# Optimization experiments

Measured on AMD Instinct MI355X. Metric: run time of the kernel, lower is better.

Reference implementation:

```python
import jax, jax.numpy as jnp
import numpy as np

D_MODEL = 1024
N_HEADS = 16
HEAD_DIM = D_MODEL // N_HEADS


def setup_inputs() -> dict:
    key = jax.random.key(0)
    ks = jax.random.split(key, 5)
    B, T = 2, 2048
    x = jax.random.normal(ks[0], (B, T, D_MODEL), dtype=jnp.float32)
    s_in = 1.0 / np.sqrt(D_MODEL)
    W_qkv = jax.random.normal(ks[1], (D_MODEL, 3 * D_MODEL), dtype=jnp.float32) * s_in
    b_qkv = jnp.zeros((3 * D_MODEL,), dtype=jnp.float32)
    W_out = jax.random.normal(ks[2], (D_MODEL, D_MODEL), dtype=jnp.float32) * s_in
    b_out = jnp.zeros((D_MODEL,), dtype=jnp.float32)
    gamma = jnp.ones((D_MODEL,), dtype=jnp.float32)
    beta = jnp.zeros((D_MODEL,), dtype=jnp.float32)
    return {"x": x, "W_qkv": W_qkv, "b_qkv": b_qkv, "W_out": W_out,
            "b_out": b_out, "gamma": gamma, "beta": beta}


def _layernorm(x, gamma, beta, eps=1e-5):
    mu = jnp.mean(x, axis=-1, keepdims=True)
    var = jnp.var(x, axis=-1, keepdims=True)
    return (x - mu) * jax.lax.rsqrt(var + eps) * gamma + beta


def reference(x, W_qkv, b_qkv, W_out, b_out, gamma, beta):
    B, T, D = x.shape
    residual = x
    h = _layernorm(x, gamma, beta)
    qkv = h @ W_qkv + b_qkv                      # [B, T, 3D]
    qkv = qkv.reshape(B, T, 3, N_HEADS, HEAD_DIM)
    q = jnp.transpose(qkv[:, :, 0], (0, 2, 1, 3))  # [B, H, T, hd]
    k = jnp.transpose(qkv[:, :, 1], (0, 2, 1, 3))
    v = jnp.transpose(qkv[:, :, 2], (0, 2, 1, 3))
    scale = 1.0 / np.sqrt(HEAD_DIM)
    attn = jnp.einsum("bhqd,bhkd->bhqk", q, k) * scale
    attn = jax.nn.softmax(attn, axis=-1)
    out = jnp.einsum("bhqk,bhkd->bhqd", attn, v)   # [B, H, T, hd]
    out = jnp.transpose(out, (0, 2, 1, 3)).reshape(B, T, D)
    out = out @ W_out + b_out
    return residual + out
```

## Files before the change

kernel.cpp:

```cpp
#include <hip/hip_runtime.h>
#include <hip/hip_bf16.h>


#define DINL static __device__ __forceinline__

typedef __attribute__((ext_vector_type(8))) short bf16x8;
typedef __attribute__((ext_vector_type(4))) float f32x4;

DINL float fast_exp2(float x) { return __builtin_amdgcn_exp2f(x); }

DINL unsigned short f2bf(float f) {
  __hip_bfloat16 h = __float2bfloat16(f);
  unsigned short u;
  __builtin_memcpy(&u, &h, 2);
  return u;
}

DINL unsigned int bfbits(float f) {
  unsigned int u;
  __builtin_memcpy(&u, &f, 4);
  return (u + 0x8000u) >> 16;
}

DINL void gload_lds16(const void* g, void* l) {
  __builtin_amdgcn_global_load_lds((__attribute__((address_space(1))) void*)g,
                                   (__attribute__((address_space(3))) void*)l,
                                   16, 0, 0);
}

__global__ __launch_bounds__(256)
void ln_kernel(const float* __restrict__ x, const float* __restrict__ gamma,
               const float* __restrict__ beta, unsigned short* __restrict__ h) {
  __shared__ float red[8];
  int row = blockIdx.x;
  int t = threadIdx.x;
  float4 v = reinterpret_cast<const float4*>(x + (size_t)row * 1024)[t];
  float s  = v.x + v.y + v.z + v.w;
  float sq = v.x*v.x + v.y*v.y + v.z*v.z + v.w*v.w;
#pragma unroll
  for (int off = 1; off < 64; off <<= 1) {
    s  += __shfl_xor(s, off);
    sq += __shfl_xor(sq, off);
  }
  int wid = t >> 6;
  if ((t & 63) == 0) { red[wid] = s; red[4 + wid] = sq; }
  __syncthreads();
  s  = red[0] + red[1] + red[2] + red[3];
  sq = red[4] + red[5] + red[6] + red[7];
  float mu   = s * (1.0f / 1024.0f);
  float var  = sq * (1.0f / 1024.0f) - mu * mu;
  float rstd = rsqrtf(var + 1e-5f);
  float4 g = reinterpret_cast<const float4*>(gamma)[t];
  float4 b = reinterpret_cast<const float4*>(beta)[t];
  ushort4 o;
  o.x = f2bf((v.x - mu) * rstd * g.x + b.x);
  o.y = f2bf((v.y - mu) * rstd * g.y + b.y);
  o.z = f2bf((v.z - mu) * rstd * g.z + b.z);
  o.w = f2bf((v.w - mu) * rstd * g.w + b.w);
  reinterpret_cast<ushort4*>(h + (size_t)row * 1024)[t] = o;
}

__global__ __launch_bounds__(256)
void transpose_cast_kernel(const float* __restrict__ src, unsigned short* __restrict__ dst,
                           int R, int C) {
  __shared__ float tile[32][33];
  int tx = threadIdx.x & 31, ty = threadIdx.x >> 5;
  int c0 = blockIdx.x * 32, r0 = blockIdx.y * 32;
#pragma unroll
  for (int i = 0; i < 4; i++)
    tile[ty + i * 8][tx] = src[(size_t)(r0 + ty + i * 8) * C + c0 + tx];
  __syncthreads();
#pragma unroll
  for (int i = 0; i < 4; i++) {
    int r = ty + i * 8;
    dst[(size_t)(c0 + r) * R + r0 + tx] = f2bf(tile[tx][r]);
  }
}

template <int BM, int MODE>
__global__ __launch_bounds__(256)
void gemm128(const unsigned short* __restrict__ A,
             const unsigned short* __restrict__ Bt,
             int K,
             const float* __restrict__ bias,
             unsigned short* __restrict__ qdst, unsigned short* __restrict__ kdst,
             unsigned short* __restrict__ vTdst,
             const float* __restrict__ xres, float* __restrict__ out) {
  static_assert(BM == 128 || BM == 64, "");
  constexpr int MR = BM / 32;
  __shared__ unsigned short As[BM * 64];
  __shared__ unsigned short Bs[8192];
  int tid = threadIdx.x, wid = tid >> 6, lane = tid & 63;
  int l15 = lane & 15, l4 = lane >> 4;
  int brow = blockIdx.y * BM, bcol = blockIdx.x * 128;
  int wr = wid >> 1, wc = wid & 1;
  f32x4 acc[MR][4] = {};

  for (int kt = 0; kt < K; kt += 64) {
    __syncthreads();
#pragma unroll
    for (int r = 0; r < MR; r++) {
      int c  = wid * (BM * 2) + r * 64;
      int cl = c + lane;
      int kb = cl / BM, row = cl % BM;
      gload_lds16(A + (size_t)(brow + row) * K + kt + kb * 8, As + c * 8);
    }
#pragma unroll
    for (int r = 0; r < 4; r++) {
      int c  = wid * 256 + r * 64;
      int cl = c + lane;
      int kb = cl >> 7, row = cl & 127;
      gload_lds16(Bt + (size_t)(bcol + row) * K + kt + kb * 8, Bs + c * 8);
    }
    __syncthreads();
#pragma unroll
    for (int ks = 0; ks < 2; ks++) {
      int kb = ks * 4 + l4;
      bf16x8 af[MR], bfr[4];
#pragma unroll
      for (int m = 0; m < MR; m++)
        af[m] = *reinterpret_cast<const bf16x8*>(As + (kb * BM + wr * (BM / 2) + m * 16 + l15) * 8);
#pragma unroll
      for (int n = 0; n < 4; n++)
        bfr[n] = *reinterpret_cast<const bf16x8*>(Bs + (kb * 128 + wc * 64 + n * 16 + l15) * 8);
#pragma unroll
      for (int m = 0; m < MR; m++)
#pragma unroll
        for (int n = 0; n < 4; n++)
          acc[m][n] = __builtin_amdgcn_mfma_f32_16x16x32_bf16(af[m], bfr[n], acc[m][n], 0, 0, 0);
    }
  }

  if (MODE == 0) {
    int sec = bcol >> 10;
    int secbase = sec << 10;
#pragma unroll
    for (int m = 0; m < MR; m++) {
      int row0 = brow + wr * (BM / 2) + m * 16 + l4 * 4;
      int b = row0 >> 11, t0 = row0 & 2047;
#pragma unroll
      for (int n = 0; n < 4; n++) {
        int col = (bcol & 1023) + wc * 64 + n * 16 + l15;
        float bv = bias[secbase + col];
        int hh = col >> 6, d = col & 63;
        if (sec == 2) {
          ushort4 pk;
          pk.x = f2bf(acc[m][n][0] + bv);
          pk.y = f2bf(acc[m][n][1] + bv);
          pk.z = f2bf(acc[m][n][2] + bv);
          pk.w = f2bf(acc[m][n][3] + bv);
          *reinterpret_cast<ushort4*>(vTdst + ((size_t)(b * 16 + hh) * 64 + d) * 2048 + t0) = pk;
        } else {
          unsigned short* dst = (sec == 0) ? qdst : kdst;
          float sc = (sec == 0) ? 0.125f * 1.44269504088896f : 1.0f;
#pragma unroll
          for (int j = 0; j < 4; j++)
            dst[((size_t)(b * 16 + hh) * 2048 + t0 + j) * 64 + d] = f2bf((acc[m][n][j] + bv) * sc);
        }
      }
    }
  } else {
#pragma unroll
    for (int m = 0; m < MR; m++) {
      int row0 = brow + wr * (BM / 2) + m * 16 + l4 * 4;
#pragma unroll
      for (int n = 0; n < 4; n++) {
        int col = bcol + wc * 64 + n * 16 + l15;
        float bv = bias[col];
#pragma unroll
        for (int j = 0; j < 4; j++) {
          size_t idx = (size_t)(row0 + j) * 1024 + col;
          out[idx] = acc[m][n][j] + bv + xres[idx];
        }
      }
    }
  }
}

__global__ __launch_bounds__(256, 2)
void attn_kernel(const unsigned short* __restrict__ q,
                 const unsigned short* __restrict__ kk,
                 const unsigned short* __restrict__ vT,
                 unsigned short* __restrict__ o) {
  const int T = 2048;
  __shared__ unsigned short Ks[2][8192];
  __shared__ unsigned short Ps[4][2][2048];
  int tid = threadIdx.x, wid = tid >> 6, lane = tid & 63;
  int l15 = lane & 15, l4 = lane >> 4;
  int swz = (l15 & 7) << 3;

  int lin = blockIdx.x;
  int rl  = (lin & 7) * 64 + (lin >> 3);
  int bx = rl & 15, bh = rl >> 4;
  int q0 = bx * 128 + wid * 32;

  const unsigned short* qh = q  + (size_t)bh * T * 64;
  const unsigned short* kh = kk + (size_t)bh * T * 64;
  const unsigned short* vh = vT + (size_t)bh * 64 * T;

  bf16x8 qf[2][2];
#pragma unroll
  for (int m = 0; m < 2; m++)
#pragma unroll
    for (int ks = 0; ks < 2; ks++)
      qf[m][ks] = *reinterpret_cast<const bf16x8*>(
          qh + (size_t)(q0 + m * 16 + l15) * 64 + ks * 32 + l4 * 8);

  f32x4 accO[2][4] = {};
  float lst[2] = {0.0f, 0.0f};

#define STAGE128(buf, kv0)                                                     \
  {                                                                            \
    _Pragma("unroll") for (int r = 0; r < 4; r++) {                            \
      int c  = (wid * 4 + r) * 64;                                             \
      int cl = c + lane;                                                       \
      int key = cl >> 3;                                                       \
      int kb  = (cl & 7) ^ (key & 7);                                          \
      gload_lds16(kh + (size_t)((kv0) + key) * 64 + kb * 8, &Ks[buf][c * 8]);  \
    }                                                                          \
  }

#define QKSM(sub, par)                                                         \
  {                                                                            \
    f32x4 s[2][4] = {};                                                        \
    __builtin_amdgcn_s_setprio(1);                                             \
    _Pragma("unroll") for (int ks = 0; ks < 2; ks++) {                         \
      _Pragma("unroll") for (int n = 0; n < 4; n++) {                          \
        int kkey = (sub) * 64 + n * 16 + l15;                                  \
        int slot = kkey * 8 + ((ks * 4 + l4) ^ (kkey & 7));                    \
        bf16x8 kf = *reinterpret_cast<const bf16x8*>(&Ks[cur][slot * 8]);      \
        _Pragma("unroll") for (int m = 0; m < 2; m++)                          \
          s[m][n] = __builtin_amdgcn_mfma_f32_16x16x32_bf16(kf, qf[m][ks],     \
                                                            s[m][n], 0, 0, 0); \
      }                                                                        \
    }                                                                          \
    __builtin_amdgcn_s_setprio(0);                                             \
    _Pragma("unroll") for (int m = 0; m < 2; m++) {                            \
      float sum = 0.0f;                                                        \
      _Pragma("unroll") for (int n = 0; n < 4; n++) {                          \
        _Pragma("unroll") for (int j = 0; j < 4; j++) {                        \
          float p = fast_exp2(s[m][n][j]);                                     \
          s[m][n][j] = p;                                                      \
          sum += p;                                                            \
        }                                                                      \
        unsigned int u0 = bfbits(s[m][n][0]) | (bfbits(s[m][n][1]) << 16);     \
        unsigned int u1 = bfbits(s[m][n][2]) | (bfbits(s[m][n][3]) << 16);     \
        *reinterpret_cast<uint2*>(                                             \
            &Ps[wid][par][(m * 16 + l15) * 64 + ((n * 16 + l4 * 4) ^ swz)]) =  \
            make_uint2(u0, u1);                                                \
      }                                                                        \
      lst[m] += sum;                                                           \
    }                                                                          \
  }

#define PV(par, vf)                                                            \
  {                                                                            \
    __builtin_amdgcn_s_setprio(1);                                             \
    _Pragma("unroll") for (int ks = 0; ks < 2; ks++) {                         \
      _Pragma("unroll") for (int m = 0; m < 2; m++) {                          \
        bf16x8 pf = *reinterpret_cast<const bf16x8*>(                          \
            &Ps[wid][par][(m * 16 + l15) * 64 + ((ks * 32 + l4 * 8) ^ swz)]);  \
        _Pragma("unroll") for (int n = 0; n < 4; n++)                          \
          accO[m][n] = __builtin_amdgcn_mfma_f32_16x16x32_bf16(                \
              vf[ks][n], pf, accO[m][n], 0, 0, 0);                             \
      }                                                                        \
    }                                                                          \
    __builtin_amdgcn_s_setprio(0);                                             \
  }

#define LOADV(vf, kvs)                                                         \
  {                                                                            \
    _Pragma("unroll") for (int ks = 0; ks < 2; ks++)                           \
      _Pragma("unroll") for (int n = 0; n < 4; n++)                            \
        vf[ks][n] = *reinterpret_cast<const bf16x8*>(                          \
            vh + (size_t)(n * 16 + l15) * T + (kvs) + ks * 32 + l4 * 8);       \
  }

  STAGE128(0, 0);
  __syncthreads();
  int cur = 0;

  for (int kv0 = 0; kv0 < T; kv0 += 128) {
    bf16x8 vf0[2][4], vf1[2][4];
    LOADV(vf0, kv0);
    LOADV(vf1, kv0 + 64);
    if (kv0 + 128 < T) STAGE128(cur ^ 1, kv0 + 128);
    QKSM(0, 0);
    QKSM(1, 1);
    PV(0, vf0);
    PV(1, vf1);
    __syncthreads();
    cur ^= 1;
  }
#undef QKSM
#undef PV
#undef LOADV
#undef STAGE128

  int b = bh >> 4, hh = bh & 15;
#pragma unroll
  for (int m = 0; m < 2; m++) {
    float l = lst[m];
    l += __shfl_xor(l, 16);
    l += __shfl_xor(l, 32);
    float inv = 1.0f / l;
    int row = q0 + m * 16 + l15;
#pragma unroll
    for (int n = 0; n < 4; n++) {
      ushort4 pk;
      pk.x = f2bf(accO[m][n][0] * inv);
      pk.y = f2bf(accO[m][n][1] * inv);
      pk.z = f2bf(accO[m][n][2] * inv);
      pk.w = f2bf(accO[m][n][3] * inv);
      *reinterpret_cast<ushort4*>(
          &o[(size_t)(b * 2048 + row) * 1024 + hh * 64 + n * 16 + l4 * 4]) = pk;
    }
  }
}

extern "C" void kernel_launch(void* const* d_in, const int* in_sizes, int n_in,
                              void* d_out, int out_size, void* d_ws, size_t ws_size,
                              hipStream_t stream) {
  const float* x     = (const float*)d_in[0];
  const float* W_qkv = (const float*)d_in[1];
  const float* b_qkv = (const float*)d_in[2];
  const float* W_out = (const float*)d_in[3];
  const float* b_out = (const float*)d_in[4];
  const float* gamma = (const float*)d_in[5];
  const float* beta  = (const float*)d_in[6];
  float* out = (float*)d_out;

  char* ws = (char*)d_ws;
  unsigned short* h     = (unsigned short*)(ws);
  unsigned short* WqkvT = (unsigned short*)(ws + (size_t)(8)  * 1024 * 1024);
  unsigned short* WoutT = (unsigned short*)(ws + (size_t)(14) * 1024 * 1024);
  unsigned short* qb    = (unsigned short*)(ws + (size_t)(16) * 1024 * 1024);
  unsigned short* kb    = (unsigned short*)(ws + (size_t)(24) * 1024 * 1024);
  unsigned short* vTb   = (unsigned short*)(ws + (size_t)(32) * 1024 * 1024);
  unsigned short* attno = (unsigned short*)(ws + (size_t)(40) * 1024 * 1024);

  ln_kernel<<<4096, 256, 0, stream>>>(x, gamma, beta, h);
  transpose_cast_kernel<<<dim3(96, 32), 256, 0, stream>>>(W_qkv, WqkvT, 1024, 3072);
  transpose_cast_kernel<<<dim3(32, 32), 256, 0, stream>>>(W_out, WoutT, 1024, 1024);
  gemm128<128, 0><<<dim3(24, 32), 256, 0, stream>>>(h, WqkvT, 1024, b_qkv, qb, kb, vTb, nullptr, nullptr);
  attn_kernel<<<512, 256, 0, stream>>>(qb, kb, vTb, attno);
  gemm128<64, 1><<<dim3(8, 64), 256, 0, stream>>>(attno, WoutT, 1024, b_out, nullptr, nullptr, nullptr, x, out);
}
```

Measured before the change: 167.8 us.

## Split attention over KV halves with a combine kernel and interleave QK/softmax/PV

Splits each attention block's key range into two halves (split-K flash-decoding style), doubling the grid to 1024 blocks, and adds a combine kernel that sums the unnormalized bf16 partial outputs and divides by the summed row sums. The inner loop is reordered so the second QK overlaps the first PV, the P buffer shrinks to one slot per wave, and the occupancy hint rises to 3 blocks per CU. It targets underfilled CUs and serialized MFMA/exp phases, at the cost of an extra launch, extra global traffic for the partials, and bf16 rounding of unnormalized partial sums. Workspace buffers are re-laid-out to alias dead buffers.

```diff
diff --git a/kernel.cpp b/kernel.cpp
--- a/kernel.cpp
+++ b/kernel.cpp
@@ -20,6 +20,13 @@
   unsigned int u;
   __builtin_memcpy(&u, &f, 4);
   return (u + 0x8000u) >> 16;
+}
+
+DINL float bf2f(unsigned short u) {
+  unsigned int x = ((unsigned int)u) << 16;
+  float f;
+  __builtin_memcpy(&f, &x, 4);
+  return f;
 }
 
 DINL void gload_lds16(const void* g, void* l) {
@@ -177,23 +184,28 @@
   }
 }
 
-__global__ __launch_bounds__(256, 2)
+__global__ __launch_bounds__(256, 3)
 void attn_kernel(const unsigned short* __restrict__ q,
                  const unsigned short* __restrict__ kk,
                  const unsigned short* __restrict__ vT,
-                 unsigned short* __restrict__ o) {
+                 unsigned short* __restrict__ opA, unsigned short* __restrict__ opB,
+                 float* __restrict__ lpA, float* __restrict__ lpB) {
   const int T = 2048;
   __shared__ unsigned short Ks[2][8192];
-  __shared__ unsigned short Ps[4][2][2048];
+  __shared__ unsigned short Ps[4][2048];
   int tid = threadIdx.x, wid = tid >> 6, lane = tid & 63;
   int l15 = lane & 15, l4 = lane >> 4;
   int swz = (l15 & 7) << 3;
 
   int lin = blockIdx.x;
-  int rl  = (lin & 7) * 64 + (lin >> 3);
-  int bx = rl & 15, bh = rl >> 4;
+  int rl  = (lin & 7) * 128 + (lin >> 3);
+  int bh = rl >> 5, rem = rl & 31;
+  int bx = rem >> 1, sp = rem & 1;
   int q0 = bx * 128 + wid * 32;
-
+  int kvbase = sp << 10;
+
+  unsigned short* op = sp ? opB : opA;
+  float* lp = sp ? lpB : lpA;
   const unsigned short* qh = q  + (size_t)bh * T * 64;
   const unsigned short* kh = kk + (size_t)bh * T * 64;
   const unsigned short* vh = vT + (size_t)bh * 64 * T;
@@ -220,9 +232,8 @@
     }                                                                          \
   }
 
-#define QKSM(sub, par)                                                         \
-  {                                                                            \
-    f32x4 s[2][4] = {};                                                        \
+#define QK(sub, sdst)                                                          \
+  {                                                                            \
     __builtin_amdgcn_s_setprio(1);                                             \
     _Pragma("unroll") for (int ks = 0; ks < 2; ks++) {                         \
       _Pragma("unroll") for (int n = 0; n < 4; n++) {                          \
@@ -230,36 +241,40 @@
         int slot = kkey * 8 + ((ks * 4 + l4) ^ (kkey & 7));                    \
         bf16x8 kf = *reinterpret_cast<const bf16x8*>(&Ks[cur][slot * 8]);      \
         _Pragma("unroll") for (int m = 0; m < 2; m++)                          \
-          s[m][n] = __builtin_amdgcn_mfma_f32_16x16x32_bf16(kf, qf[m][ks],     \
-                                                            s[m][n], 0, 0, 0); \
+          sdst[m][n] = __builtin_amdgcn_mfma_f32_16x16x32_bf16(                \
+              kf, qf[m][ks], sdst[m][n], 0, 0, 0);                             \
       }                                                                        \
     }                                                                          \
     __builtin_amdgcn_s_setprio(0);                                             \
+  }
+
+#define SM(ssrc)                                                               \
+  {                                                                            \
     _Pragma("unroll") for (int m = 0; m < 2; m++) {                            \
       float sum = 0.0f;                                                        \
       _Pragma("unroll") for (int n = 0; n < 4; n++) {                          \
         _Pragma("unroll") for (int j = 0; j < 4; j++) {                        \
-          float p = fast_exp2(s[m][n][j]);                                     \
-          s[m][n][j] = p;                                                      \
+          float p = fast_exp2(ssrc[m][n][j]);                                  \
+          ssrc[m][n][j] = p;                                                   \
           sum += p;                                                            \
         }                                                                      \
-        unsigned int u0 = bfbits(s[m][n][0]) | (bfbits(s[m][n][1]) << 16);     \
-        unsigned int u1 = bfbits(s[m][n][2]) | (bfbits(s[m][n][3]) << 16);     \
+        unsigned int u0 = bfbits(ssrc[m][n][0]) | (bfbits(ssrc[m][n][1]) << 16); \
+        unsigned int u1 = bfbits(ssrc[m][n][2]) | (bfbits(ssrc[m][n][3]) << 16); \
         *reinterpret_cast<uint2*>(                                             \
-            &Ps[wid][par][(m * 16 + l15) * 64 + ((n * 16 + l4 * 4) ^ swz)]) =  \
+            &Ps[wid][(m * 16 + l15) * 64 + ((n * 16 + l4 * 4) ^ swz)]) =       \
             make_uint2(u0, u1);                                                \
       }                                                                        \
       lst[m] += sum;                                                           \
     }                                                                          \
   }
 
-#define PV(par, vf)                                                            \
+#define PV(vf)                                                                 \
   {                                                                            \
     __builtin_amdgcn_s_setprio(1);                                             \
     _Pragma("unroll") for (int ks = 0; ks < 2; ks++) {                         \
       _Pragma("unroll") for (int m = 0; m < 2; m++) {                          \
         bf16x8 pf = *reinterpret_cast<const bf16x8*>(                          \
-            &Ps[wid][par][(m * 16 + l15) * 64 + ((ks * 32 + l4 * 8) ^ swz)]);  \
+            &Ps[wid][(m * 16 + l15) * 64 + ((ks * 32 + l4 * 8) ^ swz)]);       \
         _Pragma("unroll") for (int n = 0; n < 4; n++)                          \
           accO[m][n] = __builtin_amdgcn_mfma_f32_16x16x32_bf16(                \
               vf[ks][n], pf, accO[m][n], 0, 0, 0);                             \
@@ -276,23 +291,30 @@
             vh + (size_t)(n * 16 + l15) * T + (kvs) + ks * 32 + l4 * 8);       \
   }
 
-  STAGE128(0, 0);
+  STAGE128(0, kvbase);
   __syncthreads();
   int cur = 0;
 
-  for (int kv0 = 0; kv0 < T; kv0 += 128) {
-    bf16x8 vf0[2][4], vf1[2][4];
+  for (int r8 = 0; r8 < 8; r8++) {
+    int kv0 = kvbase + r8 * 128;
+    bf16x8 vf0[2][4];
     LOADV(vf0, kv0);
+    if (r8 + 1 < 8) STAGE128(cur ^ 1, kv0 + 128);
+    f32x4 s0[2][4] = {};
+    QK(0, s0);
+    SM(s0);
+    f32x4 s1[2][4] = {};
+    QK(1, s1);
+    PV(vf0);
+    bf16x8 vf1[2][4];
     LOADV(vf1, kv0 + 64);
-    if (kv0 + 128 < T) STAGE128(cur ^ 1, kv0 + 128);
-    QKSM(0, 0);
-    QKSM(1, 1);
-    PV(0, vf0);
-    PV(1, vf1);
+    SM(s1);
+    PV(vf1);
     __syncthreads();
     cur ^= 1;
   }
-#undef QKSM
+#undef QK
+#undef SM
 #undef PV
 #undef LOADV
 #undef STAGE128
@@ -303,19 +325,38 @@
     float l = lst[m];
     l += __shfl_xor(l, 16);
     l += __shfl_xor(l, 32);
-    float inv = 1.0f / l;
     int row = q0 + m * 16 + l15;
+    if (l4 == 0) lp[(size_t)bh * 2048 + row] = l;
 #pragma unroll
     for (int n = 0; n < 4; n++) {
       ushort4 pk;
-      pk.x = f2bf(accO[m][n][0] * inv);
-      pk.y = f2bf(accO[m][n][1] * inv);
-      pk.z = f2bf(accO[m][n][2] * inv);
-      pk.w = f2bf(accO[m][n][3] * inv);
+      pk.x = (unsigned short)bfbits(accO[m][n][0]);
+      pk.y = (unsigned short)bfbits(accO[m][n][1]);
+      pk.z = (unsigned short)bfbits(accO[m][n][2]);
+      pk.w = (unsigned short)bfbits(accO[m][n][3]);
       *reinterpret_cast<ushort4*>(
-          &o[(size_t)(b * 2048 + row) * 1024 + hh * 64 + n * 16 + l4 * 4]) = pk;
-    }
-  }
+          &op[(size_t)(b * 2048 + row) * 1024 + hh * 64 + n * 16 + l4 * 4]) = pk;
+    }
+  }
+}
+
+__global__ __launch_bounds__(256)
+void attn_combine(const unsigned short* __restrict__ opA,
+                  const unsigned short* __restrict__ opB,
+                  const float* __restrict__ lpA, const float* __restrict__ lpB,
+                  unsigned short* __restrict__ attno) {
+  int i0 = (blockIdx.x * 256 + threadIdx.x) * 8;
+  int r = i0 >> 10, c = i0 & 1023;
+  int lidx = ((r >> 11) * 16 + (c >> 6)) * 2048 + (r & 2047);
+  float inv = 1.0f / (lpA[lidx] + lpB[lidx]);
+  bf16x8 a = *reinterpret_cast<const bf16x8*>(opA + i0);
+  bf16x8 bb = *reinterpret_cast<const bf16x8*>(opB + i0);
+  bf16x8 o;
+#pragma unroll
+  for (int k = 0; k < 8; k++)
+    o[k] = (short)(unsigned short)bfbits(
+        (bf2f((unsigned short)a[k]) + bf2f((unsigned short)bb[k])) * inv);
+  *reinterpret_cast<bf16x8*>(attno + i0) = o;
 }
 
 extern "C" void kernel_launch(void* const* d_in, const int* in_sizes, int n_in,
@@ -331,18 +372,24 @@
   float* out = (float*)d_out;
 
   char* ws = (char*)d_ws;
+  const size_t MB = 1024 * 1024;
   unsigned short* h     = (unsigned short*)(ws);
-  unsigned short* WqkvT = (unsigned short*)(ws + (size_t)(8)  * 1024 * 1024);
-  unsigned short* WoutT = (unsigned short*)(ws + (size_t)(14) * 1024 * 1024);
-  unsigned short* qb    = (unsigned short*)(ws + (size_t)(16) * 1024 * 1024);
-  unsigned short* kb    = (unsigned short*)(ws + (size_t)(24) * 1024 * 1024);
-  unsigned short* vTb   = (unsigned short*)(ws + (size_t)(32) * 1024 * 1024);
-  unsigned short* attno = (unsigned short*)(ws + (size_t)(40) * 1024 * 1024);
+  unsigned short* WqkvT = (unsigned short*)(ws + 8 * MB);
+  unsigned short* opA   = (unsigned short*)(ws);
+  unsigned short* opB   = (unsigned short*)(ws + 8 * MB);
+  float*          lpA   = (float*)(ws + 16 * MB);
+  float*          lpB   = (float*)(ws + 16 * MB + 512 * 1024);
+  unsigned short* WoutT = (unsigned short*)(ws + 17 * MB);
+  unsigned short* qb    = (unsigned short*)(ws + 19 * MB);
+  unsigned short* attno = (unsigned short*)(ws + 19 * MB);
+  unsigned short* kb    = (unsigned short*)(ws + 27 * MB);
+  unsigned short* vTb   = (unsigned short*)(ws + 35 * MB);
 
   ln_kernel<<<4096, 256, 0, stream>>>(x, gamma, beta, h);
   transpose_cast_kernel<<<dim3(96, 32), 256, 0, stream>>>(W_qkv, WqkvT, 1024, 3072);
   transpose_cast_kernel<<<dim3(32, 32), 256, 0, stream>>>(W_out, WoutT, 1024, 1024);
   gemm128<128, 0><<<dim3(24, 32), 256, 0, stream>>>(h, WqkvT, 1024, b_qkv, qb, kb, vTb, nullptr, nullptr);
-  attn_kernel<<<512, 256, 0, stream>>>(qb, kb, vTb, attno);
+  attn_kernel<<<1024, 256, 0, stream>>>(qb, kb, vTb, opA, opB, lpA, lpB);
+  attn_combine<<<2048, 256, 0, stream>>>(opA, opB, lpA, lpB, attno);
   gemm128<64, 1><<<dim3(8, 64), 256, 0, stream>>>(attno, WoutT, 1024, b_out, nullptr, nullptr, nullptr, x, out);
 }
```

Measured after the change: 330.9 us. +97.2%, slower.
